# Optimization experiments

Hardware: AMD Instinct MI355X
Metric: run time of the kernel (lower is better)

The kernel has to match this reference:

```python
import jax, jax.numpy as jnp
import numpy as np

HID = 2048
NH = 16
HD = HID // NH  # 128
THETA = 10000.0


def _rope_cos_sin(position_ids):
    # inv_freq: [HD/2]
    inv_freq = 1.0 / (THETA ** (jnp.arange(0, HD, 2, dtype=jnp.float32) / HD))
    freqs = position_ids.astype(jnp.float32)[:, :, None] * inv_freq[None, None, :]  # [b,s,hd/2]
    emb = jnp.concatenate([freqs, freqs], axis=-1)  # [b,s,hd]
    return jnp.cos(emb), jnp.sin(emb)


def _rotate_half(x):
    x1, x2 = x[..., : HD // 2], x[..., HD // 2:]
    return jnp.concatenate([-x2, x1], axis=-1)


def setup_inputs() -> dict:
    key = jax.random.key(0)
    ks = jax.random.split(key, 10)
    b, s = 2, 2048
    scale = 1.0 / np.sqrt(HID)
    hidden_states = jax.random.normal(ks[0], (b, s, HID), dtype=jnp.float32)
    wq = jax.random.normal(ks[1], (HID, HID), dtype=jnp.float32) * scale
    wk = jax.random.normal(ks[2], (HID, HID), dtype=jnp.float32) * scale
    wv = jax.random.normal(ks[3], (HID, HID), dtype=jnp.float32) * scale
    wo = jax.random.normal(ks[4], (HID, HID), dtype=jnp.float32) * scale
    bq = jnp.zeros((HID,), jnp.float32)
    bk = jnp.zeros((HID,), jnp.float32)
    bv = jnp.zeros((HID,), jnp.float32)
    bo = jnp.zeros((HID,), jnp.float32)
    # HF-style additive causal mask [b,1,q,kv]: 0 on/below diag, large negative above
    neg = jnp.finfo(jnp.float32).min
    causal = jnp.where(jnp.tril(jnp.ones((s, s), dtype=bool)), 0.0, neg)
    attention_mask = jnp.broadcast_to(causal[None, None], (b, 1, s, s)).astype(jnp.float32)
    position_ids = jnp.broadcast_to(jnp.arange(s, dtype=jnp.int32)[None], (b, s))
    return {
        "hidden_states": hidden_states,
        "wq": wq, "bq": bq, "wk": wk, "bk": bk,
        "wv": wv, "bv": bv, "wo": wo, "bo": bo,
        "attention_mask": attention_mask, "position_ids": position_ids,
    }


def reference(hidden_states, wq, bq, wk, bk, wv, bv, wo, bo, attention_mask, position_ids):
    b, s, _ = hidden_states.shape
    q = hidden_states @ wq.T + bq  # [b,s,hid]
    k = hidden_states @ wk.T + bk
    v = hidden_states @ wv.T + bv
    # [b, nh, s, hd]
    q = q.reshape(b, s, NH, HD).transpose(0, 2, 1, 3)
    k = k.reshape(b, s, NH, HD).transpose(0, 2, 1, 3)
    v = v.reshape(b, s, NH, HD).transpose(0, 2, 1, 3)
    cos, sin = _rope_cos_sin(position_ids)  # [b,s,hd]
    cos, sin = cos[:, None], sin[:, None]  # unsqueeze_dim=1 -> [b,1,s,hd]
    q = q * cos + _rotate_half(q) * sin
    k = k * cos + _rotate_half(k) * sin
    scores = jnp.einsum("bhqd,bhkd->bhqk", q, k) / np.sqrt(HD)
    scores = scores + attention_mask
    attn = jax.nn.softmax(scores.astype(jnp.float32), axis=-1).astype(q.dtype)
    out = jnp.einsum("bhqk,bhkd->bhqd", attn, v)  # [b,nh,s,hd]
    out = out.transpose(0, 2, 1, 3).reshape(b, s, HID)
    return out @ wo.T + bo
```

## Files before the change

kernel.cpp:

```cpp
#include <hip/hip_runtime.h>

#define S_LEN 2048
#define HID   2048
#define NHEAD 16
#define HDIM  128
#define BATCH 2
#define KDIM  2048

using bf16x8  = __attribute__((ext_vector_type(8))) short;
using f32x4   = __attribute__((ext_vector_type(4))) float;
using f32x16  = __attribute__((ext_vector_type(16))) float;
using short4v = __attribute__((ext_vector_type(4))) short;
using uint4v  = __attribute__((ext_vector_type(4))) unsigned;

__device__ __forceinline__ short f2bf(float f) {
  union { float f; unsigned u; } v; v.f = f;
  unsigned r = v.u + 0x7fffu + ((v.u >> 16) & 1u);
  return (short)(r >> 16);
}
__device__ __forceinline__ float bf2f(short s) {
  union { unsigned u; float f; } v;
  v.u = ((unsigned)(unsigned short)s) << 16;
  return v.f;
}

__device__ __forceinline__ void gl_lds16(const void* g, void* l) {
  __builtin_amdgcn_global_load_lds(
      (const __attribute__((address_space(1))) void*)g,
      (__attribute__((address_space(3))) void*)l, 16, 0, 0);
}

__global__ __launch_bounds__(256)
void convert_all(const float* __restrict__ hs, const float* __restrict__ wq,
                 const float* __restrict__ wk, const float* __restrict__ wv,
                 const float* __restrict__ wo,
                 short* __restrict__ hsb, short* __restrict__ wqkv,
                 short* __restrict__ wob)
{
  const int base = blockIdx.x * 256 + threadIdx.x;
#pragma unroll
  for (int it = 0; it < 6; ++it) {
    int j = base + it * 524288;
    const float* src; short* dst;
    if (j < 1048576)      { src = hs; dst = hsb; }
    else if (j < 1572864) { j -= 1048576; src = wq; dst = wqkv; }
    else if (j < 2097152) { j -= 1572864; src = wk; dst = wqkv + 4194304; }
    else if (j < 2621440) { j -= 2097152; src = wv; dst = wqkv + 8388608; }
    else                  { j -= 2621440; src = wo; dst = wob; }
    f32x4 a = ((const f32x4*)src)[2 * j];
    f32x4 b = ((const f32x4*)src)[2 * j + 1];
    bf16x8 o;
    o[0]=f2bf(a[0]); o[1]=f2bf(a[1]); o[2]=f2bf(a[2]); o[3]=f2bf(a[3]);
    o[4]=f2bf(b[0]); o[5]=f2bf(b[1]); o[6]=f2bf(b[2]); o[7]=f2bf(b[3]);
    ((bf16x8*)dst)[j] = o;
  }
}

template<int KIND>
__global__ __launch_bounds__(256)
void gemm128(const short* __restrict__ A, const short* __restrict__ B,
             const float* __restrict__ bias0, const float* __restrict__ bias1,
             const float* __restrict__ bias2,
             void* __restrict__ O0, void* __restrict__ O1, void* __restrict__ O2)
{
  __shared__ __align__(16) short As[128 * 64];
  __shared__ __align__(16) short Bs[128 * 64];
  const int tid  = threadIdx.x;
  const int lane = tid & 63, wave = tid >> 6;
  const int ln = lane & 15, g = lane >> 4;
  const int wr = wave >> 1, wc = wave & 1;
  const int m0 = blockIdx.x * 128, n0 = blockIdx.y * 128;

  const int srow   = tid >> 3;
  const int schunk = (tid & 7) ^ (srow & 7);
  const short* aS = A + (size_t)(m0 + srow) * KDIM + schunk * 8;
  const short* bS = B + (size_t)(n0 + srow) * KDIM + schunk * 8;

  f32x4 acc[4][4] = {};

  for (int k0 = 0; k0 < KDIM; k0 += 64) {
    __syncthreads();
#pragma unroll
    for (int j = 0; j < 4; ++j) {
      gl_lds16(aS + k0 + j * (32 * KDIM), &As[j * 2048 + tid * 8]);
      gl_lds16(bS + k0 + j * (32 * KDIM), &Bs[j * 2048 + tid * 8]);
    }
    __syncthreads();

#pragma unroll
    for (int ks = 0; ks < 2; ++ks) {
      bf16x8 af[4], bfm[4];
#pragma unroll
      for (int i = 0; i < 4; ++i) {
        const int r = wr * 64 + i * 16 + ln;
        af[i] = *(const bf16x8*)&As[r * 64 + (((ks * 4 + g) ^ (r & 7)) << 3)];
      }
#pragma unroll
      for (int j2 = 0; j2 < 4; ++j2) {
        const int r = wc * 64 + j2 * 16 + ln;
        bfm[j2] = *(const bf16x8*)&Bs[r * 64 + (((ks * 4 + g) ^ (r & 7)) << 3)];
      }
#pragma unroll
      for (int i = 0; i < 4; ++i)
#pragma unroll
        for (int j2 = 0; j2 < 4; ++j2)
          acc[i][j2] = __builtin_amdgcn_mfma_f32_16x16x32_bf16(af[i], bfm[j2], acc[i][j2], 0, 0, 0);
    }
  }

  if constexpr (KIND == 0) {
    const int seg   = n0 >> 11;
    const int nbase = (n0 & 2047) + wc * 64;
    const float* bias = (seg == 0) ? bias0 : (seg == 1) ? bias1 : bias2;
    float bvv[4];
#pragma unroll
    for (int j = 0; j < 4; ++j) bvv[j] = bias[nbase + j * 16 + ln];
    if (seg < 2) {
      short* C = (short*)(seg ? O1 : O0);
#pragma unroll
      for (int i = 0; i < 4; ++i) {
        const int mb = m0 + wr * 64 + i * 16 + 4 * g;
#pragma unroll
        for (int j = 0; j < 4; ++j) {
          const int nl = nbase + j * 16 + ln;
          const int h = nl >> 7, d = nl & 127;
#pragma unroll
          for (int e = 0; e < 4; ++e) {
            const int m = mb + e, bb = m >> 11, t = m & (S_LEN - 1);
            C[((size_t)((bb * NHEAD + h) * S_LEN + t) << 7) + d] = f2bf(acc[i][j][e] + bvv[j]);
          }
        }
      }
    } else {
      short* C = (short*)O2;
#pragma unroll
      for (int i = 0; i < 4; ++i) {
        const int mb = m0 + wr * 64 + i * 16 + 4 * g;
        const int bb = mb >> 11, t0 = mb & (S_LEN - 1);
#pragma unroll
        for (int j = 0; j < 4; ++j) {
          const int nl = nbase + j * 16 + ln;
          const int h = nl >> 7, d = nl & 127;
          short4v v;
#pragma unroll
          for (int e = 0; e < 4; ++e) v[e] = f2bf(acc[i][j][e] + bvv[j]);
          *(short4v*)&C[((size_t)((bb * NHEAD + h) * HDIM + d)) * S_LEN + t0] = v;
        }
      }
    }
  } else {
    float* C = (float*)O0;
    float bvv[4];
#pragma unroll
    for (int j = 0; j < 4; ++j) bvv[j] = bias0[n0 + wc * 64 + j * 16 + ln];
#pragma unroll
    for (int i = 0; i < 4; ++i) {
      const int mb = m0 + wr * 64 + i * 16 + 4 * g;
#pragma unroll
      for (int j = 0; j < 4; ++j) {
        const int n = n0 + wc * 64 + j * 16 + ln;
#pragma unroll
        for (int e = 0; e < 4; ++e)
          C[(size_t)(mb + e) * HID + n] = acc[i][j][e] + bvv[j];
      }
    }
  }
}

#define QSCALE 0.12752767502f
__global__ __launch_bounds__(256)
void rope_kernel(short* __restrict__ Qb, short* __restrict__ Kb,
                 const int* __restrict__ pos_ids)
{
  const int row = blockIdx.x * 4 + (threadIdx.x >> 6);
  const int d   = threadIdx.x & 63;
  const int bh  = row >> 11, t = row & (S_LEN - 1);
  const int b   = bh >> 4;
  const float pos = (float)pos_ids[b * S_LEN + t];
  const float inv = exp2f((float)d * -0.20762050593f);
  float s, c;
  sincosf(pos * inv, &s, &c);
  const size_t base = (size_t)row * HDIM;
  {
    float x1 = bf2f(Qb[base + d]), x2 = bf2f(Qb[base + d + 64]);
    Qb[base + d]      = f2bf((x1 * c - x2 * s) * QSCALE);
    Qb[base + d + 64] = f2bf((x2 * c + x1 * s) * QSCALE);
  }
  {
    float x1 = bf2f(Kb[base + d]), x2 = bf2f(Kb[base + d + 64]);
    Kb[base + d]      = f2bf(x1 * c - x2 * s);
    Kb[base + d + 64] = f2bf(x2 * c + x1 * s);
  }
}

__global__ __launch_bounds__(256, 2)
void attn_kernel(const short* __restrict__ Qb, const short* __restrict__ Kb,
                 const short* __restrict__ Vt, short* __restrict__ AO)
{
  __shared__ __align__(16) short Ks[128 * 128];
  __shared__ __align__(16) short Vs[128 * 128];
  const int tid  = threadIdx.x;
  const int wave = tid >> 6, lane = tid & 63;
  const int lq = lane & 31, lh = lane >> 5;
  const int bid = blockIdx.x;
  const int bh  = bid & 31;
  const int grp = bid >> 5;
  const int yt  = (grp & 7) ^ ((grp & 8) ? 15 : 0);
  const int qw  = yt * 128 + wave * 32;
  const int q   = qw + lq;

  const short* Kbh = Kb + (size_t)bh * (S_LEN * HDIM);
  const short* Vbh = Vt + (size_t)bh * (S_LEN * HDIM);
  const int sw   = ((tid & 15) ^ ((tid >> 4) & 7)) << 3;
  const int kOff = (tid >> 4) * HDIM + sw;
  const int vOff = (tid >> 4) * S_LEN + sw;

  bf16x8 qf[8];
#pragma unroll
  for (int kk = 0; kk < 8; ++kk)
    qf[kk] = *(const bf16x8*)&Qb[((size_t)bh * S_LEN + q) * HDIM + kk * 16 + lh * 8];

  f32x16 o[4] = {};
  float m_s = -3.0e38f, l_s = 0.f;

  for (int kvt = 0; kvt <= yt; ++kvt) {
    const int kv0 = kvt * 128;
    __syncthreads();
#pragma unroll
    for (int p = 0; p < 8; ++p) {
      gl_lds16(Kbh + (size_t)kv0 * HDIM + kOff + p * (16 * HDIM), &Ks[p * 2048 + tid * 8]);
      gl_lds16(Vbh + kv0 + vOff + p * (16 * S_LEN),               &Vs[p * 2048 + tid * 8]);
    }
    __syncthreads();

    f32x16 sfr[4] = {};
    __builtin_amdgcn_s_setprio(1);
#pragma unroll
    for (int kk = 0; kk < 8; ++kk) {
#pragma unroll
      for (int nt = 0; nt < 4; ++nt) {
        const int row = nt * 32 + lq;
        bf16x8 ak = *(const bf16x8*)&Ks[(row * 128 + kk * 16 + lh * 8) ^ ((row & 7) << 3)];
        sfr[nt] = __builtin_amdgcn_mfma_f32_32x32x16_bf16(ak, qf[kk], sfr[nt], 0, 0, 0);
      }
    }
    __builtin_amdgcn_s_setprio(0);

    if (kvt == yt) {
#pragma unroll
      for (int nt = 0; nt < 4; ++nt) {
        const int kvb = kv0 + nt * 32 + 4 * lh;
#pragma unroll
        for (int r = 0; r < 16; ++r) {
          const int kv = kvb + (r & 3) + 8 * (r >> 2);
          if (kv > q) sfr[nt][r] = -3.0e38f;
        }
      }
    }

    float rmax = -3.0e38f;
#pragma unroll
    for (int nt = 0; nt < 4; ++nt)
#pragma unroll
      for (int r = 0; r < 16; ++r) rmax = fmaxf(rmax, sfr[nt][r]);
    rmax = fmaxf(rmax, __shfl_xor(rmax, 32));

    if (__any(rmax > m_s + 8.0f)) {
      const float nm = fmaxf(m_s, rmax);
      const float corr = exp2f(m_s - nm);
      m_s = nm;
      l_s *= corr;
#pragma unroll
      for (int dt = 0; dt < 4; ++dt)
#pragma unroll
        for (int r = 0; r < 16; ++r) o[dt][r] *= corr;
    }

    float ps = 0.f;
#pragma unroll
    for (int nt = 0; nt < 4; ++nt)
#pragma unroll
      for (int r = 0; r < 16; ++r) {
        const float pv = exp2f(sfr[nt][r] - m_s);
        sfr[nt][r] = pv;
        ps += pv;
      }
    l_s += ps;

    bf16x8 pa[8];
#pragma unroll
    for (int kk = 0; kk < 8; ++kk) {
      const int nt = kk >> 1, c8 = (kk & 1) * 8;
      unsigned w0, w1, w2, w3;
      asm("v_cvt_pk_bf16_f32 %0, %1, %2" : "=v"(w0) : "v"(sfr[nt][c8 + 0]), "v"(sfr[nt][c8 + 1]));
      asm("v_cvt_pk_bf16_f32 %0, %1, %2" : "=v"(w1) : "v"(sfr[nt][c8 + 2]), "v"(sfr[nt][c8 + 3]));
      asm("v_cvt_pk_bf16_f32 %0, %1, %2" : "=v"(w2) : "v"(sfr[nt][c8 + 4]), "v"(sfr[nt][c8 + 5]));
      asm("v_cvt_pk_bf16_f32 %0, %1, %2" : "=v"(w3) : "v"(sfr[nt][c8 + 6]), "v"(sfr[nt][c8 + 7]));
      asm volatile("v_permlane32_swap_b32 %0, %1" : "+v"(w0), "+v"(w2));
      asm volatile("v_permlane32_swap_b32 %0, %1" : "+v"(w1), "+v"(w3));
      uint4v u; u[0] = w0; u[1] = w1; u[2] = w2; u[3] = w3;
      pa[kk] = __builtin_bit_cast(bf16x8, u);
    }

    __builtin_amdgcn_s_setprio(1);
#pragma unroll
    for (int kk = 0; kk < 8; ++kk) {
#pragma unroll
      for (int dt = 0; dt < 4; ++dt) {
        const int row = dt * 32 + lq;
        bf16x8 av = *(const bf16x8*)&Vs[(row * 128 + kk * 16 + lh * 8) ^ ((row & 7) << 3)];
        o[dt] = __builtin_amdgcn_mfma_f32_32x32x16_bf16(av, pa[kk], o[dt], 0, 0, 0);
      }
    }
    __builtin_amdgcn_s_setprio(0);
  }

  l_s += __shfl_xor(l_s, 32);
  const float inv = 1.0f / l_s;
  const int b = bh >> 4, hh = bh & 15;
  short* dst = &AO[((size_t)b * S_LEN + q) * HID + hh * HDIM];
#pragma unroll
  for (int dt = 0; dt < 4; ++dt) {
#pragma unroll
    for (int rq = 0; rq < 4; ++rq) {
      short4v v4;
#pragma unroll
      for (int e = 0; e < 4; ++e) v4[e] = f2bf(o[dt][rq * 4 + e] * inv);
      *(short4v*)&dst[dt * 32 + rq * 8 + 4 * lh] = v4;
    }
  }
}

extern "C" void kernel_launch(void* const* d_in, const int* in_sizes, int n_in,
                              void* d_out, int out_size, void* d_ws, size_t ws_size,
                              hipStream_t stream)
{
  const float* hs = (const float*)d_in[0];
  const float* wq = (const float*)d_in[1];
  const float* bq = (const float*)d_in[2];
  const float* wk = (const float*)d_in[3];
  const float* bk = (const float*)d_in[4];
  const float* wv = (const float*)d_in[5];
  const float* bv = (const float*)d_in[6];
  const float* wo = (const float*)d_in[7];
  const float* bo = (const float*)d_in[8];
  const int*  pos = (const int*)d_in[10];
  float* out = (float*)d_out;

  const size_t TSZ = (size_t)BATCH * NHEAD * S_LEN * HDIM;
  short* Qb   = (short*)d_ws;
  short* Kb   = Qb + TSZ;
  short* Vt   = Kb + TSZ;
  short* hsb  = Vt + TSZ;
  short* AO   = hsb;
  short* Wqkv = hsb + TSZ;
  short* wob  = Wqkv + 12582912;

  convert_all<<<2048, 256, 0, stream>>>(hs, wq, wk, wv, wo, hsb, Wqkv, wob);
  gemm128<0><<<dim3(32, 48), 256, 0, stream>>>(hsb, Wqkv, bq, bk, bv, Qb, Kb, Vt);
  rope_kernel<<<(BATCH * NHEAD * S_LEN) / 4, 256, 0, stream>>>(Qb, Kb, pos);
  attn_kernel<<<512, 256, 0, stream>>>(Qb, Kb, Vt, AO);
  gemm128<1><<<dim3(32, 16), 256, 0, stream>>>(AO, wob, bo, nullptr, nullptr, out, nullptr, nullptr);
}
```

Measured before the change: 248.9 us.

## Replace QKV projection GEMM with 256x256 tile, 8-wave double-buffered pipelined kernel

Swaps the fused QKV projection from a 128x128-tile, 4-wave GEMM to a new 256x256-tile, 512-thread kernel. It double-buffers LDS, splits the A and B global-to-LDS prefetch across sub-phases, and interleaves barriers with s_setprio around the MFMA bursts. The larger tiles roughly halve global traffic per FLOP, and the explicit schedule is meant to overlap loads with matrix math. The cost is 128KB of LDS and heavy register use per block. Only 384 blocks are launched, so occupancy and tail effects may suffer.

```diff
diff --git a/kernel.cpp b/kernel.cpp
--- a/kernel.cpp
+++ b/kernel.cpp
@@ -56,6 +56,160 @@
   }
 }
 
+__global__ __launch_bounds__(512)
+void gemm256_8p(const short* __restrict__ A, const short* __restrict__ B,
+                const float* __restrict__ bq, const float* __restrict__ bkb,
+                const float* __restrict__ bv,
+                short* __restrict__ Qo, short* __restrict__ Ko,
+                short* __restrict__ Vo)
+{
+  __shared__ __align__(16) short LA[2 * 16384];
+  __shared__ __align__(16) short LB[2 * 16384];
+  const int tid  = threadIdx.x;
+  const int lane = tid & 63, wave = tid >> 6;
+  const int ln = lane & 15, g = lane >> 4;
+  const int wm = wave >> 2, wn = wave & 3;
+  const int m0 = blockIdx.x * 256, n0 = blockIdx.y * 256;
+
+  const int srow   = tid >> 3;
+  const int schunk = (tid & 7) ^ (srow & 7);
+  const short* aS = A + (size_t)(m0 + srow) * KDIM + schunk * 8;
+  const short* bS = B + (size_t)(n0 + srow) * KDIM + schunk * 8;
+
+  const int rAb = wm * 128 + ln;
+  const int rBb = wn * 64 + ln;
+  const int ax = rAb & 7, bx2 = rBb & 7;
+
+  f32x4 acc[8][4] = {};
+
+  auto stA2 = [&](int T, int s, int h) {
+    gl_lds16(aS + (size_t)(h * 128)      * KDIM + T * 64,
+             &LA[s * 16384 + h * 8192 + tid * 8]);
+    gl_lds16(aS + (size_t)(h * 128 + 64) * KDIM + T * 64,
+             &LA[s * 16384 + h * 8192 + 4096 + tid * 8]);
+  };
+  auto stB2 = [&](int T, int s, int h) {
+    gl_lds16(bS + (size_t)(h * 128)      * KDIM + T * 64,
+             &LB[s * 16384 + h * 8192 + tid * 8]);
+    gl_lds16(bS + (size_t)(h * 128 + 64) * KDIM + T * 64,
+             &LB[s * 16384 + h * 8192 + 4096 + tid * 8]);
+  };
+  auto AF = [&](int s, int mf, int ks) {
+    const int r = rAb + mf * 16;
+    return *(const bf16x8*)&LA[s * 16384 + r * 64 + (((ks * 4 + g) ^ ax) << 3)];
+  };
+  auto BFr = [&](int s, int nf, int ks) {
+    const int r = rBb + nf * 16;
+    return *(const bf16x8*)&LB[s * 16384 + r * 64 + (((ks * 4 + g) ^ bx2) << 3)];
+  };
+
+  stA2(0, 0, 0); stA2(0, 0, 1); stB2(0, 0, 0); stB2(0, 0, 1);
+
+#define TILE8(T, VMC, STG)                                                     \
+  {                                                                            \
+    const int cur_ = (T) & 1, nxt_ = cur_ ^ 1;                                 \
+    bf16x8 bfr[4], af[4];                                                      \
+     \
+    if (STG) { stA2((T) + 1, nxt_, 0); stA2((T) + 1, nxt_, 1); }               \
+    asm volatile("s_waitcnt vmcnt(" #VMC ")" ::: "memory");                    \
+    __builtin_amdgcn_s_barrier();                                              \
+    __builtin_amdgcn_sched_barrier(0);                                         \
+    _Pragma("unroll") for (int nf = 0; nf < 4; ++nf) bfr[nf] = BFr(cur_, nf, 0); \
+    _Pragma("unroll") for (int m = 0; m < 4; ++m)  af[m]  = AF(cur_, m, 0);    \
+    __builtin_amdgcn_s_setprio(1);                                             \
+    _Pragma("unroll") for (int m = 0; m < 4; ++m)                              \
+      _Pragma("unroll") for (int nf = 0; nf < 4; ++nf)                         \
+        acc[m][nf] = __builtin_amdgcn_mfma_f32_16x16x32_bf16(                  \
+            af[m], bfr[nf], acc[m][nf], 0, 0, 0);                              \
+    __builtin_amdgcn_s_setprio(0);                                             \
+    __builtin_amdgcn_sched_barrier(0);                                         \
+    __builtin_amdgcn_s_barrier();                                              \
+           \
+    if (STG) { stB2((T) + 1, nxt_, 0); stB2((T) + 1, nxt_, 1); }               \
+    _Pragma("unroll") for (int m = 0; m < 4; ++m) af[m] = AF(cur_, 4 + m, 0);  \
+    __builtin_amdgcn_s_barrier();                                              \
+    __builtin_amdgcn_sched_barrier(0);                                         \
+    __builtin_amdgcn_s_setprio(1);                                             \
+    _Pragma("unroll") for (int m = 0; m < 4; ++m)                              \
+      _Pragma("unroll") for (int nf = 0; nf < 4; ++nf)                         \
+        acc[4 + m][nf] = __builtin_amdgcn_mfma_f32_16x16x32_bf16(              \
+            af[m], bfr[nf], acc[4 + m][nf], 0, 0, 0);                          \
+    __builtin_amdgcn_s_setprio(0);                                             \
+    __builtin_amdgcn_sched_barrier(0);                                         \
+    __builtin_amdgcn_s_barrier();                                              \
+                                    \
+    _Pragma("unroll") for (int nf = 0; nf < 4; ++nf) bfr[nf] = BFr(cur_, nf, 1); \
+    _Pragma("unroll") for (int m = 0; m < 4; ++m)  af[m]  = AF(cur_, m, 1);    \
+    __builtin_amdgcn_s_barrier();                                              \
+    __builtin_amdgcn_sched_barrier(0);                                         \
+    __builtin_amdgcn_s_setprio(1);                                             \
+    _Pragma("unroll") for (int m = 0; m < 4; ++m)                              \
+      _Pragma("unroll") for (int nf = 0; nf < 4; ++nf)                         \
+        acc[m][nf] = __builtin_amdgcn_mfma_f32_16x16x32_bf16(                  \
+            af[m], bfr[nf], acc[m][nf], 0, 0, 0);                              \
+    __builtin_amdgcn_s_setprio(0);                                             \
+    __builtin_amdgcn_sched_barrier(0);                                         \
+    __builtin_amdgcn_s_barrier();                                              \
+                                    \
+    _Pragma("unroll") for (int m = 0; m < 4; ++m) af[m] = AF(cur_, 4 + m, 1);  \
+    __builtin_amdgcn_s_barrier();                                              \
+    __builtin_amdgcn_sched_barrier(0);                                         \
+    __builtin_amdgcn_s_setprio(1);                                             \
+    _Pragma("unroll") for (int m = 0; m < 4; ++m)                              \
+      _Pragma("unroll") for (int nf = 0; nf < 4; ++nf)                         \
+        acc[4 + m][nf] = __builtin_amdgcn_mfma_f32_16x16x32_bf16(              \
+            af[m], bfr[nf], acc[4 + m][nf], 0, 0, 0);                          \
+    __builtin_amdgcn_s_setprio(0);                                             \
+    __builtin_amdgcn_sched_barrier(0);                                         \
+    __builtin_amdgcn_s_barrier();                                              \
+  }
+
+  for (int T = 0; T < 31; ++T) TILE8(T, 4, true)
+  TILE8(31, 0, false)
+#undef TILE8
+
+  const int seg   = blockIdx.y >> 3;
+  const int nbase = (n0 & 2047) + wn * 64;
+  const float* bias = (seg == 0) ? bq : (seg == 1) ? bkb : bv;
+  float bvv[4];
+#pragma unroll
+  for (int nf = 0; nf < 4; ++nf) bvv[nf] = bias[nbase + nf * 16 + ln];
+
+  if (seg < 2) {
+    short* C = seg ? Ko : Qo;
+#pragma unroll
+    for (int mf = 0; mf < 8; ++mf) {
+      const int mb = m0 + wm * 128 + mf * 16 + 4 * g;
+      const int bb = mb >> 11, t = mb & (S_LEN - 1);
+#pragma unroll
+      for (int nf = 0; nf < 4; ++nf) {
+        const int nl = nbase + nf * 16 + ln;
+        const int h = nl >> 7, d = nl & 127;
+#pragma unroll
+        for (int e = 0; e < 4; ++e)
+          C[((size_t)((bb * NHEAD + h) * S_LEN + t + e) << 7) + d] =
+              f2bf(acc[mf][nf][e] + bvv[nf]);
+      }
+    }
+  } else {
+    short* C = Vo;
+#pragma unroll
+    for (int mf = 0; mf < 8; ++mf) {
+      const int mb = m0 + wm * 128 + mf * 16 + 4 * g;
+      const int bb = mb >> 11, t0 = mb & (S_LEN - 1);
+#pragma unroll
+      for (int nf = 0; nf < 4; ++nf) {
+        const int nl = nbase + nf * 16 + ln;
+        const int h = nl >> 7, d = nl & 127;
+        short4v v;
+#pragma unroll
+        for (int e = 0; e < 4; ++e) v[e] = f2bf(acc[mf][nf][e] + bvv[nf]);
+        *(short4v*)&C[((size_t)((bb * NHEAD + h) * HDIM + d)) * S_LEN + t0] = v;
+      }
+    }
+  }
+}
+
 template<int KIND>
 __global__ __launch_bounds__(256)
 void gemm128(const short* __restrict__ A, const short* __restrict__ B,
@@ -108,47 +262,7 @@
     }
   }
 
-  if constexpr (KIND == 0) {
-    const int seg   = n0 >> 11;
-    const int nbase = (n0 & 2047) + wc * 64;
-    const float* bias = (seg == 0) ? bias0 : (seg == 1) ? bias1 : bias2;
-    float bvv[4];
-#pragma unroll
-    for (int j = 0; j < 4; ++j) bvv[j] = bias[nbase + j * 16 + ln];
-    if (seg < 2) {
-      short* C = (short*)(seg ? O1 : O0);
-#pragma unroll
-      for (int i = 0; i < 4; ++i) {
-        const int mb = m0 + wr * 64 + i * 16 + 4 * g;
-#pragma unroll
-        for (int j = 0; j < 4; ++j) {
-          const int nl = nbase + j * 16 + ln;
-          const int h = nl >> 7, d = nl & 127;
-#pragma unroll
-          for (int e = 0; e < 4; ++e) {
-            const int m = mb + e, bb = m >> 11, t = m & (S_LEN - 1);
-            C[((size_t)((bb * NHEAD + h) * S_LEN + t) << 7) + d] = f2bf(acc[i][j][e] + bvv[j]);
-          }
-        }
-      }
-    } else {
-      short* C = (short*)O2;
-#pragma unroll
-      for (int i = 0; i < 4; ++i) {
-        const int mb = m0 + wr * 64 + i * 16 + 4 * g;
-        const int bb = mb >> 11, t0 = mb & (S_LEN - 1);
-#pragma unroll
-        for (int j = 0; j < 4; ++j) {
-          const int nl = nbase + j * 16 + ln;
-          const int h = nl >> 7, d = nl & 127;
-          short4v v;
-#pragma unroll
-          for (int e = 0; e < 4; ++e) v[e] = f2bf(acc[i][j][e] + bvv[j]);
-          *(short4v*)&C[((size_t)((bb * NHEAD + h) * HDIM + d)) * S_LEN + t0] = v;
-        }
-      }
-    }
-  } else {
+  if constexpr (KIND == 1) {
     float* C = (float*)O0;
     float bvv[4];
 #pragma unroll
@@ -357,7 +471,7 @@
   short* wob  = Wqkv + 12582912;
 
   convert_all<<<2048, 256, 0, stream>>>(hs, wq, wk, wv, wo, hsb, Wqkv, wob);
-  gemm128<0><<<dim3(32, 48), 256, 0, stream>>>(hsb, Wqkv, bq, bk, bv, Qb, Kb, Vt);
+  gemm256_8p<<<dim3(16, 24), 512, 0, stream>>>(hsb, Wqkv, bq, bk, bv, Qb, Kb, Vt);
   rope_kernel<<<(BATCH * NHEAD * S_LEN) / 4, 256, 0, stream>>>(Qb, Kb, pos);
   attn_kernel<<<512, 256, 0, stream>>>(Qb, Kb, Vt, AO);
   gemm128<1><<<dim3(32, 16), 256, 0, stream>>>(AO, wob, bo, nullptr, nullptr, out, nullptr, nullptr);
```

Result: slower. 287.5 us (+15.5%).
